# Performance work log

Hardware: AMD Instinct MI355X
Metric: run time of the kernel (lower is better)

The kernel has to match this reference:

```python
import jax, jax.numpy as jnp
import numpy as np
from jax import lax

B, S, T = 128, 1000, 256
V, E, KV, H = 30, 256, 256, 512


def setup_inputs() -> dict:
    ks = jax.random.split(jax.random.key(0), 20)
    sc = 0.1
    emb = jax.random.normal(ks[0], (V, E), jnp.float32) * sc
    emb = emb.at[29].set(0.0)  # padding_idx=29
    return {
        "enc_key": jax.random.normal(ks[1], (B, S, KV), jnp.float32),
        "value": jax.random.normal(ks[2], (B, S, KV), jnp.float32),
        "y": jax.random.randint(ks[3], (T, B), 0, V),
        "encoder_len": jax.random.randint(ks[4], (B,), 1, S + 1),
        "embedding": emb,
        "W_ih1": jax.random.normal(ks[5], (4 * H, E + KV), jnp.float32) * sc,
        "b_ih1": jax.random.normal(ks[6], (4 * H,), jnp.float32) * sc,
        "W_hh1": jax.random.normal(ks[7], (4 * H, H), jnp.float32) * sc,
        "b_hh1": jax.random.normal(ks[8], (4 * H,), jnp.float32) * sc,
        "W_ih2": jax.random.normal(ks[9], (4 * H, H), jnp.float32) * sc,
        "b_ih2": jax.random.normal(ks[10], (4 * H,), jnp.float32) * sc,
        "W_hh2": jax.random.normal(ks[11], (4 * H, H), jnp.float32) * sc,
        "b_hh2": jax.random.normal(ks[12], (4 * H,), jnp.float32) * sc,
        "Wq": jax.random.normal(ks[13], (KV, H), jnp.float32) * sc,
        "bq": jax.random.normal(ks[14], (KV,), jnp.float32) * sc,
        "Wc": jax.random.normal(ks[15], (V, 2 * KV), jnp.float32) * sc,
        "bc": jax.random.normal(ks[16], (V,), jnp.float32) * sc,
    }


def _lstm_cell(x, h, c, W_ih, b_ih, W_hh, b_hh):
    gates = x @ W_ih.T + b_ih + h @ W_hh.T + b_hh
    i, f, g, o = jnp.split(gates, 4, axis=1)
    c_new = jax.nn.sigmoid(f) * c + jax.nn.sigmoid(i) * jnp.tanh(g)
    h_new = jax.nn.sigmoid(o) * jnp.tanh(c_new)
    return h_new, c_new


def reference(enc_key, value, y, encoder_len, embedding,
              W_ih1, b_ih1, W_hh1, b_hh1,
              W_ih2, b_ih2, W_hh2, b_hh2,
              Wq, bq, Wc, bc):
    # y: [T, B] -> [B, T]; note: original computes mask from encoder_len but the
    # non-in-place masked_fill discards it, so masking has NO effect (reproduced).
    del encoder_len
    yT = y.T  # [B, T]
    b, s, kv = enc_key.shape
    scale = jnp.sqrt(jnp.asarray(s, jnp.float32))
    char_embeds = embedding[yT]          # [B, T, E]
    ctx0 = value.mean(axis=1)            # [B, KV]  (value.permute(0,2,1).mean(-1))
    h = W_hh1.shape[1]
    z = jnp.zeros((b, h), enc_key.dtype)

    def step(carry, e_t):
        h1, c1, h2, c2, ctx = carry
        x = jnp.concatenate([e_t, ctx], axis=1)                 # [B, E+KV]
        h1n, c1n = _lstm_cell(x, h1, c1, W_ih1, b_ih1, W_hh1, b_hh1)
        # original feeds lstm1's CELL state into lstm2 (hidden_states[0][1])
        h2n, c2n = _lstm_cell(c1n, h2, c2, W_ih2, b_ih2, W_hh2, b_hh2)
        # query from lstm2's CELL state (hidden_states[1][1])
        q = c2n @ Wq.T + bq                                     # [B, KV]
        energy = (jnp.einsum('bsk,bk->bs', enc_key, q) + 1e-9) / scale
        attn = jax.nn.softmax(energy, axis=1)                   # [B, S]
        ctxn = jnp.einsum('bsk,bs->bk', value, attn)            # [B, KV]
        pred = jnp.concatenate([ctxn, q], axis=1) @ Wc.T + bc   # [B, V]
        return (h1n, c1n, h2n, c2n, ctxn), (pred, attn[0])

    _, (preds, attn0) = lax.scan(step, (z, z, z, z, ctx0),
                                 jnp.swapaxes(char_embeds, 0, 1))
    predictions = jnp.transpose(preds, (1, 0, 2)).reshape(b, -1)  # [B, T*V] (cat dim=1)
    attentions = attn0[..., None]                                 # [T, S, 1]
    return predictions, attentions
```

## Files before the change

kernel.cpp:

```cpp
#include <hip/hip_runtime.h>
#include <hip/hip_bf16.h>

#define NB 128
#define NS 1000
#define NSH 500
#define NT 256
#define NV 30
#define NE 256
#define NKV 256
#define NH 512
#define NG 2048
#define NK 1024

typedef __hip_bfloat16 bf;
typedef unsigned short ushortT;

__device__ __forceinline__ float sigm(float x){ return 1.f/(1.f+__expf(-x)); }
__device__ __forceinline__ float tanh_fast(float x){ float e=__expf(2.f*x); return 1.f - 2.f/(e+1.f); }
__device__ __forceinline__ float bf2f(ushortT u){ return __uint_as_float(((unsigned)u)<<16); }
__device__ __forceinline__ void bf8_to_f(const ushortT* p, float* o){
  uint4 u = *reinterpret_cast<const uint4*>(p);
  o[0]=__uint_as_float(u.x<<16); o[1]=__uint_as_float(u.x&0xffff0000u);
  o[2]=__uint_as_float(u.y<<16); o[3]=__uint_as_float(u.y&0xffff0000u);
  o[4]=__uint_as_float(u.z<<16); o[5]=__uint_as_float(u.z&0xffff0000u);
  o[6]=__uint_as_float(u.w<<16); o[7]=__uint_as_float(u.w&0xffff0000u);
}
__device__ __forceinline__ float ldDual(const void* p, size_t i, bool bfm){
  return bfm ? bf2f(((const ushortT*)p)[i]) : ((const float*)p)[i];
}

__global__ void k_probe(const unsigned* __restrict__ x, unsigned* __restrict__ flag){
  __shared__ int cnt;
  if (threadIdx.x==0) cnt = 0;
  __syncthreads();
  int c = 0;
  #pragma unroll
  for (int i=0;i<4;++i){
    unsigned d = x[(size_t)threadIdx.x*4 + i];
    unsigned e = (d >> 7) & 0xffu;
    c += (e >= 119 && e <= 135) ? 1 : 0;
  }
  atomicAdd(&cnt, c);
  __syncthreads();
  if (threadIdx.x==0) *flag = (cnt >= 512) ? 1u : 0u;
}

__global__ void k_wtp(const void* __restrict__ A, const void* __restrict__ Bm,
                      float* __restrict__ Wtp, const unsigned* __restrict__ flag){
  const bool bfm = (*flag != 0);
  int idx = blockIdx.x*256 + threadIdx.x;
  int k = idx >> 11, pc = idx & (NG-1);
  int j = pc >> 2, g = pc & 3;
  int col = g*NH + j;
  const void* p = (k < NH) ? A : Bm;
  Wtp[idx] = ldDual(p, (size_t)col*NH + (k & (NH-1)), bfm);
}

__global__ void k_biasp(const void* bi1, const void* bh1, const void* bi2, const void* bh2,
                        float* __restrict__ bsum1, float* __restrict__ bsum2,
                        const unsigned* __restrict__ flag){
  const bool bfm = (*flag != 0);
  int idx = blockIdx.x*256 + threadIdx.x;
  int which = idx >= NG; int pc = idx & (NG-1);
  int j = pc >> 2, g = pc & 3;
  int col = g*NH + j;
  const void* a = which ? bi2 : bi1;
  const void* c = which ? bh2 : bh1;
  float v = ldDual(a, col, bfm) + ldDual(c, col, bfm);
  (which ? bsum2 : bsum1)[pc] = v;
}

__global__ void k_init(const void* __restrict__ value, const int* __restrict__ y,
                       const void* __restrict__ emb,
                       float* __restrict__ X1a, float* __restrict__ X2a,
                       float* __restrict__ c1, float* __restrict__ c2,
                       const unsigned* __restrict__ flag){
  const bool bfm = (*flag != 0);
  int b = blockIdx.x, tid = threadIdx.x;
  float acc = 0.f;
  if (bfm){
    const ushortT* vcol = (const ushortT*)value + (size_t)b*NS*NKV + tid;
    for (int s=0;s<NS;++s) acc += bf2f(vcol[(size_t)s*NKV]);
  } else {
    const float* vcol = (const float*)value + (size_t)b*NS*NKV + tid;
    for (int s=0;s<NS;++s) acc += vcol[(size_t)s*NKV];
  }
  X1a[(size_t)b*NK + NE + tid] = acc * (1.f/NS);
  int yv = y[b];
  X1a[(size_t)b*NK + tid] = ldDual(emb, (size_t)yv*NE + tid, bfm);
  X1a[(size_t)b*NK + 512 + tid] = 0.f; X1a[(size_t)b*NK + 768 + tid] = 0.f;
  X2a[(size_t)b*NK + 512 + tid] = 0.f; X2a[(size_t)b*NK + 768 + tid] = 0.f;
  c1[(size_t)b*NH + tid] = 0.f; c1[(size_t)b*NH + 256 + tid] = 0.f;
  c2[(size_t)b*NH + tid] = 0.f; c2[(size_t)b*NH + 256 + tid] = 0.f;
}

__global__ __launch_bounds__(512) void k_lstm(
    const float* __restrict__ X, const float* __restrict__ Wtp,
    const float* __restrict__ bsump,
    float* __restrict__ cstate,
    float* __restrict__ outC, int outCstride, int hasC,
    float* __restrict__ outH)
{
  const int i = blockIdx.x;
  const int cb = ((i & 7) << 3) | ((i >> 3) & 7);
  const int rb = i >> 6;
  const int r0 = rb * 32;
  const int pc0 = cb * 32;
  const int tid = threadIdx.x;
  const int khalf = tid >> 8;
  const int t8 = tid & 255;
  const int rp = t8 >> 4;
  const int cp = t8 & 15;
  __shared__ float Xs[2][64][33];
  __shared__ float redbuf[256][4];
  __shared__ float gbuf[32][33];

  float a00=0.f, a01=0.f, a10=0.f, a11=0.f;
  const int kbase = khalf * 512;
  const int sr  = t8 >> 4;
  const int sk4 = (t8 & 15) * 4;

  for (int cch = 0; cch < 8; ++cch){
    __syncthreads();
    {
      const float4 v0 = *reinterpret_cast<const float4*>(
          X + (size_t)(r0+sr)*NK + kbase + cch*64 + sk4);
      const float4 v1 = *reinterpret_cast<const float4*>(
          X + (size_t)(r0+sr+16)*NK + kbase + cch*64 + sk4);
      Xs[khalf][sk4+0][sr]    = v0.x; Xs[khalf][sk4+1][sr]    = v0.y;
      Xs[khalf][sk4+2][sr]    = v0.z; Xs[khalf][sk4+3][sr]    = v0.w;
      Xs[khalf][sk4+0][sr+16] = v1.x; Xs[khalf][sk4+1][sr+16] = v1.y;
      Xs[khalf][sk4+2][sr+16] = v1.z; Xs[khalf][sk4+3][sr+16] = v1.w;
    }
    __syncthreads();
    const float* wp = Wtp + (size_t)(kbase + cch*64)*NG + pc0 + cp*2;
    #pragma unroll 8
    for (int kk=0; kk<64; ++kk){
      const float2 w = *reinterpret_cast<const float2*>(wp + (size_t)kk*NG);
      const float2 x = *reinterpret_cast<const float2*>(&Xs[khalf][kk][rp*2]);
      a00 = fmaf(x.x, w.x, a00); a01 = fmaf(x.x, w.y, a01);
      a10 = fmaf(x.y, w.x, a10); a11 = fmaf(x.y, w.y, a11);
    }
  }
  if (khalf == 1){
    redbuf[t8][0]=a00; redbuf[t8][1]=a01; redbuf[t8][2]=a10; redbuf[t8][3]=a11;
  }
  __syncthreads();
  if (khalf == 0){
    a00 += redbuf[t8][0]; a01 += redbuf[t8][1];
    a10 += redbuf[t8][2]; a11 += redbuf[t8][3];
    gbuf[rp*2+0][cp*2+0]=a00; gbuf[rp*2+0][cp*2+1]=a01;
    gbuf[rp*2+1][cp*2+0]=a10; gbuf[rp*2+1][cp*2+1]=a11;
  }
  __syncthreads();
  if (tid < 256){
    const int er = tid >> 3;
    const int jj = tid & 7;
    const int r = r0 + er;
    const int jg = cb*8 + jj;
    const int pb = pc0 + jj*4;
    float iv = gbuf[er][jj*4+0] + bsump[pb+0];
    float fv = gbuf[er][jj*4+1] + bsump[pb+1];
    float gv = gbuf[er][jj*4+2] + bsump[pb+2];
    float ov = gbuf[er][jj*4+3] + bsump[pb+3];
    float cold = cstate[(size_t)r*NH + jg];
    float cn = sigm(fv)*cold + sigm(iv)*tanh_fast(gv);
    float hn = sigm(ov)*tanh_fast(cn);
    cstate[(size_t)r*NH + jg] = cn;
    if (hasC) outC[(size_t)r*outCstride + jg] = cn;
    outH[(size_t)r*NK + jg] = hn;
  }
}

__global__ __launch_bounds__(512) void k_attn_part(
    const float* __restrict__ c2, const void* __restrict__ Wq, const void* __restrict__ bq,
    const void* __restrict__ key, const void* __restrict__ val,
    float* __restrict__ qbuf, float* __restrict__ pctx, float* __restrict__ pstat,
    float* __restrict__ psbuf,
    const unsigned* __restrict__ flag)
{
  const bool bfm = (*flag != 0);
  const int b = blockIdx.x >> 1, half = blockIdx.x & 1;
  const int sbase = half * NSH;
  const int tid = threadIdx.x, lane = tid & 63, wave = tid >> 6;
  __shared__ float c2s[NH];
  __shared__ float qs[NKV];
  __shared__ float ps[512];
  __shared__ float red[16];
  __shared__ float ctxpart[8][NKV];

  c2s[tid] = c2[(size_t)b*NH + tid];
  __syncthreads();

  if (tid < NKV){
    float qacc = ldDual(bq, tid, bfm);
    if (bfm){
      const ushortT* wrow = (const ushortT*)Wq + (size_t)tid*NH;
      #pragma unroll 4
      for (int j=0;j<NH;j+=8){
        float wv[8]; bf8_to_f(wrow + j, wv);
        #pragma unroll
        for (int u=0;u<8;++u) qacc = fmaf(wv[u], c2s[j+u], qacc);
      }
    } else {
      const float4* wrow = reinterpret_cast<const float4*>((const float*)Wq + (size_t)tid*NH);
      #pragma unroll 4
      for (int j4=0; j4<NH/4; ++j4){
        float4 w = wrow[j4]; int j = j4*4;
        qacc = fmaf(w.x, c2s[j+0], qacc); qacc = fmaf(w.y, c2s[j+1], qacc);
        qacc = fmaf(w.z, c2s[j+2], qacc); qacc = fmaf(w.w, c2s[j+3], qacc);
      }
    }
    qs[tid] = qacc;
    if (half == 0) qbuf[(size_t)b*NKV + tid] = qacc;
  }
  __syncthreads();

  const int k0 = (lane & 15)*16;
  float qreg[16];
  #pragma unroll
  for (int u=0;u<16;++u) qreg[u] = qs[k0+u];
  const float rscale = 0.031622776601683794f;
  for (int i0 = wave*8; i0 < NSH; i0 += 64){
    int sA = i0 + (lane >> 4);
    int sB = sA + 4;
    float aA = 0.f, aB = 0.f;
    if (bfm){
      if (sA < NSH){
        const ushortT* kp = (const ushortT*)key + ((size_t)b*NS + sbase + sA)*NKV + k0;
        float xv[8];
        bf8_to_f(kp, xv);
        #pragma unroll
        for (int u=0;u<8;++u) aA = fmaf(xv[u], qreg[u], aA);
        bf8_to_f(kp + 8, xv);
        #pragma unroll
        for (int u=0;u<8;++u) aA = fmaf(xv[u], qreg[8+u], aA);
      }
      if (sB < NSH){
        const ushortT* kp = (const ushortT*)key + ((size_t)b*NS + sbase + sB)*NKV + k0;
        float xv[8];
        bf8_to_f(kp, xv);
        #pragma unroll
        for (int u=0;u<8;++u) aB = fmaf(xv[u], qreg[u], aB);
        bf8_to_f(kp + 8, xv);
        #pragma unroll
        for (int u=0;u<8;++u) aB = fmaf(xv[u], qreg[8+u], aB);
      }
    } else {
      const float* kA = (const float*)key + ((size_t)b*NS + sbase + sA)*NKV + k0;
      const float* kB = (const float*)key + ((size_t)b*NS + sbase + sB)*NKV + k0;
      float4 a0,a1,a2,a3, b0,b1,b2,b3;
      bool gA = (sA < NSH), gB = (sB < NSH);
      if (gA){
        a0 = *reinterpret_cast<const float4*>(kA);
        a1 = *reinterpret_cast<const float4*>(kA+4);
        a2 = *reinterpret_cast<const float4*>(kA+8);
        a3 = *reinterpret_cast<const float4*>(kA+12);
      }
      if (gB){
        b0 = *reinterpret_cast<const float4*>(kB);
        b1 = *reinterpret_cast<const float4*>(kB+4);
        b2 = *reinterpret_cast<const float4*>(kB+8);
        b3 = *reinterpret_cast<const float4*>(kB+12);
      }
      if (gA){
        aA = fmaf(a0.x,qreg[0],aA); aA = fmaf(a0.y,qreg[1],aA);
        aA = fmaf(a0.z,qreg[2],aA); aA = fmaf(a0.w,qreg[3],aA);
        aA = fmaf(a1.x,qreg[4],aA); aA = fmaf(a1.y,qreg[5],aA);
        aA = fmaf(a1.z,qreg[6],aA); aA = fmaf(a1.w,qreg[7],aA);
        aA = fmaf(a2.x,qreg[8],aA); aA = fmaf(a2.y,qreg[9],aA);
        aA = fmaf(a2.z,qreg[10],aA); aA = fmaf(a2.w,qreg[11],aA);
        aA = fmaf(a3.x,qreg[12],aA); aA = fmaf(a3.y,qreg[13],aA);
        aA = fmaf(a3.z,qreg[14],aA); aA = fmaf(a3.w,qreg[15],aA);
      }
      if (gB){
        aB = fmaf(b0.x,qreg[0],aB); aB = fmaf(b0.y,qreg[1],aB);
        aB = fmaf(b0.z,qreg[2],aB); aB = fmaf(b0.w,qreg[3],aB);
        aB = fmaf(b1.x,qreg[4],aB); aB = fmaf(b1.y,qreg[5],aB);
        aB = fmaf(b1.z,qreg[6],aB); aB = fmaf(b1.w,qreg[7],aB);
        aB = fmaf(b2.x,qreg[8],aB); aB = fmaf(b2.y,qreg[9],aB);
        aB = fmaf(b2.z,qreg[10],aB); aB = fmaf(b2.w,qreg[11],aB);
        aB = fmaf(b3.x,qreg[12],aB); aB = fmaf(b3.y,qreg[13],aB);
        aB = fmaf(b3.z,qreg[14],aB); aB = fmaf(b3.w,qreg[15],aB);
      }
    }
    aA += __shfl_xor(aA,1); aA += __shfl_xor(aA,2);
    aA += __shfl_xor(aA,4); aA += __shfl_xor(aA,8);
    aB += __shfl_xor(aB,1); aB += __shfl_xor(aB,2);
    aB += __shfl_xor(aB,4); aB += __shfl_xor(aB,8);
    if ((lane & 15) == 0){
      if (sA < NSH) ps[sA] = (aA + 1e-9f)*rscale;
      if (sB < NSH) ps[sB] = (aB + 1e-9f)*rscale;
    }
  }
  __syncthreads();

  float m = -1e30f;
  if (tid < NSH) m = ps[tid];
  #pragma unroll
  for (int d=1; d<64; d<<=1) m = fmaxf(m, __shfl_xor(m, d));
  if (lane == 0) red[wave] = m;
  __syncthreads();
  m = red[0];
  #pragma unroll
  for (int w=1; w<8; ++w) m = fmaxf(m, red[w]);
  float sum = 0.f;
  if (tid < NSH){ float p = __expf(ps[tid]-m); ps[tid] = p; sum = p; }
  #pragma unroll
  for (int d=1; d<64; d<<=1) sum += __shfl_xor(sum, d);
  if (lane == 0) red[8+wave] = sum;
  __syncthreads();
  sum = red[8];
  #pragma unroll
  for (int w=1; w<8; ++w) sum += red[8+w];
  if (tid == 0){
    pstat[((size_t)b*2 + half)*2 + 0] = m;
    pstat[((size_t)b*2 + half)*2 + 1] = sum;
  }
  if (b == 0 && tid < NSH) psbuf[sbase + tid] = ps[tid];

  {
    float ca[8] = {0.f,0.f,0.f,0.f,0.f,0.f,0.f,0.f};
    float cb2[8] = {0.f,0.f,0.f,0.f,0.f,0.f,0.f,0.f};
    const int sset = lane >> 5;
    const int kc = (lane & 31) * 8;
    const int sst = wave*2 + sset;
    int s = sst;
    if (bfm){
      const ushortT* vbase = (const ushortT*)val + ((size_t)b*NS + sbase)*NKV + kc;
      for (; s + 16 < NSH; s += 32){
        float p0 = ps[s], p1 = ps[s+16];
        float xv[8];
        bf8_to_f(vbase + (size_t)s*NKV, xv);
        #pragma unroll
        for (int u=0;u<8;++u) ca[u] = fmaf(xv[u], p0, ca[u]);
        bf8_to_f(vbase + (size_t)(s+16)*NKV, xv);
        #pragma unroll
        for (int u=0;u<8;++u) cb2[u] = fmaf(xv[u], p1, cb2[u]);
      }
      if (s < NSH){
        float p0 = ps[s];
        float xv[8]; bf8_to_f(vbase + (size_t)s*NKV, xv);
        #pragma unroll
        for (int u=0;u<8;++u) ca[u] = fmaf(xv[u], p0, ca[u]);
      }
    } else {
      const float* vbase = (const float*)val + ((size_t)b*NS + sbase)*NKV + kc;
      for (; s + 16 < NSH; s += 32){
        float p0 = ps[s], p1 = ps[s+16];
        const float4 v0 = *reinterpret_cast<const float4*>(vbase + (size_t)s*NKV);
        const float4 v1 = *reinterpret_cast<const float4*>(vbase + (size_t)s*NKV + 4);
        const float4 w0 = *reinterpret_cast<const float4*>(vbase + (size_t)(s+16)*NKV);
        const float4 w1 = *reinterpret_cast<const float4*>(vbase + (size_t)(s+16)*NKV + 4);
        ca[0]=fmaf(v0.x,p0,ca[0]); ca[1]=fmaf(v0.y,p0,ca[1]);
        ca[2]=fmaf(v0.z,p0,ca[2]); ca[3]=fmaf(v0.w,p0,ca[3]);
        ca[4]=fmaf(v1.x,p0,ca[4]); ca[5]=fmaf(v1.y,p0,ca[5]);
        ca[6]=fmaf(v1.z,p0,ca[6]); ca[7]=fmaf(v1.w,p0,ca[7]);
        cb2[0]=fmaf(w0.x,p1,cb2[0]); cb2[1]=fmaf(w0.y,p1,cb2[1]);
        cb2[2]=fmaf(w0.z,p1,cb2[2]); cb2[3]=fmaf(w0.w,p1,cb2[3]);
        cb2[4]=fmaf(w1.x,p1,cb2[4]); cb2[5]=fmaf(w1.y,p1,cb2[5]);
        cb2[6]=fmaf(w1.z,p1,cb2[6]); cb2[7]=fmaf(w1.w,p1,cb2[7]);
      }
      if (s < NSH){
        float p0 = ps[s];
        const float4 v0 = *reinterpret_cast<const float4*>(vbase + (size_t)s*NKV);
        const float4 v1 = *reinterpret_cast<const float4*>(vbase + (size_t)s*NKV + 4);
        ca[0]=fmaf(v0.x,p0,ca[0]); ca[1]=fmaf(v0.y,p0,ca[1]);
        ca[2]=fmaf(v0.z,p0,ca[2]); ca[3]=fmaf(v0.w,p0,ca[3]);
        ca[4]=fmaf(v1.x,p0,ca[4]); ca[5]=fmaf(v1.y,p0,ca[5]);
        ca[6]=fmaf(v1.z,p0,ca[6]); ca[7]=fmaf(v1.w,p0,ca[7]);
      }
    }
    #pragma unroll
    for (int u=0;u<8;++u){
      float v = ca[u] + cb2[u];
      v += __shfl_xor(v, 32);
      if (lane < 32) ctxpart[wave][kc+u] = v;
    }
  }
  __syncthreads();
  if (tid < NKV){
    float ctxv = 0.f;
    #pragma unroll
    for (int w=0; w<8; ++w) ctxv += ctxpart[w][tid];
    pctx[((size_t)b*2 + half)*NKV + tid] = ctxv;
  }
}

__global__ __launch_bounds__(256) void k_attn_comb(
    const float* __restrict__ qbuf, const float* __restrict__ pctx,
    const float* __restrict__ pstat, const float* __restrict__ psbuf,
    const void* __restrict__ Wc, const void* __restrict__ bc,
    const int* __restrict__ y, const void* __restrict__ emb,
    float* __restrict__ X1next, void* __restrict__ outp,
    const unsigned* __restrict__ flag, int t)
{
  const bool bfm = (*flag != 0);
  const int b = blockIdx.x, tid = threadIdx.x;
  __shared__ float qs[NKV];
  __shared__ float ctxs[NKV];
  __shared__ float psum[NV][9];

  const float mA = pstat[((size_t)b*2+0)*2+0], sA = pstat[((size_t)b*2+0)*2+1];
  const float mB = pstat[((size_t)b*2+1)*2+0], sB = pstat[((size_t)b*2+1)*2+1];
  const float m = fmaxf(mA, mB);
  const float wA = __expf(mA - m), wB = __expf(mB - m);
  const float invS = 1.f / (sA*wA + sB*wB);

  qs[tid] = qbuf[(size_t)b*NKV + tid];
  float ctxv = (pctx[((size_t)b*2+0)*NKV + tid]*wA +
                pctx[((size_t)b*2+1)*NKV + tid]*wB) * invS;
  ctxs[tid] = ctxv;
  X1next[(size_t)b*NK + NE + tid] = ctxv;

  const size_t ATTN_OFF = (size_t)NB*NT*NV;
  if (b == 0){
    for (int s=tid; s<NS; s+=256){
      float v = psbuf[s] * ((s < NSH) ? wA : wB) * invS;
      if (bfm) ((bf*)outp)[ATTN_OFF + (size_t)t*NS + s] = __float2bfloat16(v);
      else     ((float*)outp)[ATTN_OFF + (size_t)t*NS + s] = v;
    }
  }
  __syncthreads();

  {
    int vIdx = tid >> 3, part = tid & 7;
    if (vIdx < NV){
      float a = 0.f;
      int kb0 = part*64;
      for (int k=kb0; k<kb0+64; ++k){
        float xv = (k < NKV) ? ctxs[k] : qs[k-NKV];
        a = fmaf(xv, ldDual(Wc, (size_t)vIdx*(2*NKV) + k, bfm), a);
      }
      psum[vIdx][part] = a;
    }
  }
  __syncthreads();
  if (tid < NV){
    float a = ldDual(bc, tid, bfm);
    #pragma unroll
    for (int p=0;p<8;++p) a += psum[tid][p];
    size_t oi = (size_t)b*(NT*NV) + (size_t)t*NV + tid;
    if (bfm) ((bf*)outp)[oi] = __float2bfloat16(a);
    else     ((float*)outp)[oi] = a;
  }

  if (t + 1 < NT){
    int yv = y[(size_t)(t+1)*NB + b];
    X1next[(size_t)b*NK + tid] = ldDual(emb, (size_t)yv*NE + tid, bfm);
  }
}

extern "C" void kernel_launch(void* const* d_in, const int* in_sizes, int n_in,
                              void* d_out, int out_size, void* d_ws, size_t ws_size,
                              hipStream_t stream)
{
  const void* enc_key = d_in[0];
  const void* value   = d_in[1];
  const int*  y       = (const int*)d_in[2];
  const void* emb     = d_in[4];
  const void* W_ih1   = d_in[5];
  const void* b_ih1   = d_in[6];
  const void* W_hh1   = d_in[7];
  const void* b_hh1   = d_in[8];
  const void* W_ih2   = d_in[9];
  const void* b_ih2   = d_in[10];
  const void* W_hh2   = d_in[11];
  const void* b_hh2   = d_in[12];
  const void* Wq      = d_in[13];
  const void* bq      = d_in[14];
  const void* Wc      = d_in[15];
  const void* bc      = d_in[16];

  char* base = (char*)d_ws; size_t off = 0;
  auto alloc = [&](size_t bytes)->char*{
    char* p = base + off; off += (bytes + 255) & ~(size_t)255; return p;
  };
  float* Wtp1 = (float*)alloc((size_t)NK*NG*4);
  float* Wtp2 = (float*)alloc((size_t)NK*NG*4);
  float* bsum1 = (float*)alloc((size_t)NG*4);
  float* bsum2 = (float*)alloc((size_t)NG*4);
  float* X1[2] = {(float*)alloc((size_t)NB*NK*4), (float*)alloc((size_t)NB*NK*4)};
  float* X2[2] = {(float*)alloc((size_t)NB*NK*4), (float*)alloc((size_t)NB*NK*4)};
  float* c1 = (float*)alloc((size_t)NB*NH*4);
  float* c2 = (float*)alloc((size_t)NB*NH*4);
  float* qbuf  = (float*)alloc((size_t)NB*NKV*4);
  float* pctx  = (float*)alloc((size_t)NB*2*NKV*4);
  float* pstat = (float*)alloc((size_t)NB*2*2*4);
  float* psbuf = (float*)alloc((size_t)NS*4);
  unsigned* flag = (unsigned*)alloc(256);
  (void)ws_size;

  k_probe<<<1, 256, 0, stream>>>((const unsigned*)enc_key, flag);
  k_wtp<<<(NK*NG)/256, 256, 0, stream>>>(W_ih1, W_hh1, Wtp1, flag);
  k_wtp<<<(NK*NG)/256, 256, 0, stream>>>(W_ih2, W_hh2, Wtp2, flag);
  k_biasp<<<(2*NG)/256, 256, 0, stream>>>(b_ih1, b_hh1, b_ih2, b_hh2, bsum1, bsum2, flag);
  k_init<<<NB, 256, 0, stream>>>(value, y, emb, X1[0], X2[0], c1, c2, flag);

  for (int t=0; t<NT; ++t){
    int cur = t & 1, nxt = cur ^ 1;
    k_lstm<<<256, 512, 0, stream>>>(X1[cur], Wtp1, bsum1, c1,
                                    X2[cur], NK, 1, X1[nxt] + NH);
    k_lstm<<<256, 512, 0, stream>>>(X2[cur], Wtp2, bsum2, c2,
                                    nullptr, 0, 0, X2[nxt] + NH);
    k_attn_part<<<2*NB, 512, 0, stream>>>(c2, Wq, bq, enc_key, value,
                                          qbuf, pctx, pstat, psbuf, flag);
    k_attn_comb<<<NB, 256, 0, stream>>>(qbuf, pctx, pstat, psbuf, Wc, bc,
                                        y, emb, X1[nxt], d_out, flag, t);
  }
}
```

Measured before the change: 38.53 ms.

## Fuse attention combine into partial kernel via last-block atomic counter

Merges the attention combine kernel into the split-S attention kernel. Each of the two half-blocks per batch row increments a per-step atomic counter, and the second finisher merges the partial softmax stats, context and prediction. This removes one kernel launch per timestep (256 launches) and the qbuf round trip, at the cost of threadfences, an atomic, and a zeroed counter buffer sized per step.

```diff
diff --git a/kernel.cpp b/kernel.cpp
--- a/kernel.cpp
+++ b/kernel.cpp
@@ -43,6 +43,11 @@
   atomicAdd(&cnt, c);
   __syncthreads();
   if (threadIdx.x==0) *flag = (cnt >= 512) ? 1u : 0u;
+}
+
+__global__ void k_zero(unsigned* __restrict__ p, int n){
+  int i = blockIdx.x*256 + threadIdx.x;
+  if (i < n) p[i] = 0u;
 }
 
 __global__ void k_wtp(const void* __restrict__ A, const void* __restrict__ Bm,
@@ -172,12 +177,15 @@
   }
 }
 
-__global__ __launch_bounds__(512) void k_attn_part(
+__global__ __launch_bounds__(512) void k_attn(
     const float* __restrict__ c2, const void* __restrict__ Wq, const void* __restrict__ bq,
     const void* __restrict__ key, const void* __restrict__ val,
-    float* __restrict__ qbuf, float* __restrict__ pctx, float* __restrict__ pstat,
-    float* __restrict__ psbuf,
-    const unsigned* __restrict__ flag)
+    float* __restrict__ pctx, float* __restrict__ pstat, float* __restrict__ psbuf,
+    unsigned* __restrict__ cnt,
+    const void* __restrict__ Wc, const void* __restrict__ bc,
+    const int* __restrict__ y, const void* __restrict__ emb,
+    float* __restrict__ X1next, void* __restrict__ outp,
+    const unsigned* __restrict__ flag, int t)
 {
   const bool bfm = (*flag != 0);
   const int b = blockIdx.x >> 1, half = blockIdx.x & 1;
@@ -188,6 +196,9 @@
   __shared__ float ps[512];
   __shared__ float red[16];
   __shared__ float ctxpart[8][NKV];
+  __shared__ float ctxs[NKV];
+  __shared__ float psum[NV][9];
+  __shared__ unsigned oldv;
 
   c2s[tid] = c2[(size_t)b*NH + tid];
   __syncthreads();
@@ -212,7 +223,6 @@
       }
     }
     qs[tid] = qacc;
-    if (half == 0) qbuf[(size_t)b*NKV + tid] = qacc;
   }
   __syncthreads();
 
@@ -250,20 +260,20 @@
       const float* kA = (const float*)key + ((size_t)b*NS + sbase + sA)*NKV + k0;
       const float* kB = (const float*)key + ((size_t)b*NS + sbase + sB)*NKV + k0;
       float4 a0,a1,a2,a3, b0,b1,b2,b3;
-      bool gA = (sA < NSH), gB = (sB < NSH);
-      if (gA){
+      bool okA = (sA < NSH), okB = (sB < NSH);
+      if (okA){
         a0 = *reinterpret_cast<const float4*>(kA);
         a1 = *reinterpret_cast<const float4*>(kA+4);
         a2 = *reinterpret_cast<const float4*>(kA+8);
         a3 = *reinterpret_cast<const float4*>(kA+12);
       }
-      if (gB){
+      if (okB){
         b0 = *reinterpret_cast<const float4*>(kB);
         b1 = *reinterpret_cast<const float4*>(kB+4);
         b2 = *reinterpret_cast<const float4*>(kB+8);
         b3 = *reinterpret_cast<const float4*>(kB+12);
       }
-      if (gA){
+      if (okA){
         aA = fmaf(a0.x,qreg[0],aA); aA = fmaf(a0.y,qreg[1],aA);
         aA = fmaf(a0.z,qreg[2],aA); aA = fmaf(a0.w,qreg[3],aA);
         aA = fmaf(a1.x,qreg[4],aA); aA = fmaf(a1.y,qreg[5],aA);
@@ -273,7 +283,7 @@
         aA = fmaf(a3.x,qreg[12],aA); aA = fmaf(a3.y,qreg[13],aA);
         aA = fmaf(a3.z,qreg[14],aA); aA = fmaf(a3.w,qreg[15],aA);
       }
-      if (gB){
+      if (okB){
         aB = fmaf(b0.x,qreg[0],aB); aB = fmaf(b0.y,qreg[1],aB);
         aB = fmaf(b0.z,qreg[2],aB); aB = fmaf(b0.w,qreg[3],aB);
         aB = fmaf(b1.x,qreg[4],aB); aB = fmaf(b1.y,qreg[5],aB);
@@ -385,36 +395,29 @@
     for (int w=0; w<8; ++w) ctxv += ctxpart[w][tid];
     pctx[((size_t)b*2 + half)*NKV + tid] = ctxv;
   }
-}
-
-__global__ __launch_bounds__(256) void k_attn_comb(
-    const float* __restrict__ qbuf, const float* __restrict__ pctx,
-    const float* __restrict__ pstat, const float* __restrict__ psbuf,
-    const void* __restrict__ Wc, const void* __restrict__ bc,
-    const int* __restrict__ y, const void* __restrict__ emb,
-    float* __restrict__ X1next, void* __restrict__ outp,
-    const unsigned* __restrict__ flag, int t)
-{
-  const bool bfm = (*flag != 0);
-  const int b = blockIdx.x, tid = threadIdx.x;
-  __shared__ float qs[NKV];
-  __shared__ float ctxs[NKV];
-  __shared__ float psum[NV][9];
+  __syncthreads();
+
+  __threadfence();
+  if (tid == 0) oldv = atomicAdd(&cnt[b], 1u);
+  __syncthreads();
+  if (oldv != 1u) return;
+  __threadfence();
 
   const float mA = pstat[((size_t)b*2+0)*2+0], sA = pstat[((size_t)b*2+0)*2+1];
   const float mB = pstat[((size_t)b*2+1)*2+0], sB = pstat[((size_t)b*2+1)*2+1];
-  const float m = fmaxf(mA, mB);
-  const float wA = __expf(mA - m), wB = __expf(mB - m);
+  const float mm = fmaxf(mA, mB);
+  const float wA = __expf(mA - mm), wB = __expf(mB - mm);
   const float invS = 1.f / (sA*wA + sB*wB);
 
-  qs[tid] = qbuf[(size_t)b*NKV + tid];
-  float ctxv = (pctx[((size_t)b*2+0)*NKV + tid]*wA +
-                pctx[((size_t)b*2+1)*NKV + tid]*wB) * invS;
-  ctxs[tid] = ctxv;
-  X1next[(size_t)b*NK + NE + tid] = ctxv;
+  if (tid < NKV){
+    float ctxv = (pctx[((size_t)b*2+0)*NKV + tid]*wA +
+                  pctx[((size_t)b*2+1)*NKV + tid]*wB) * invS;
+    ctxs[tid] = ctxv;
+    X1next[(size_t)b*NK + NE + tid] = ctxv;
+  }
 
   const size_t ATTN_OFF = (size_t)NB*NT*NV;
-  if (b == 0){
+  if (b == 0 && tid < 256){
     for (int s=tid; s<NS; s+=256){
       float v = psbuf[s] * ((s < NSH) ? wA : wB) * invS;
       if (bfm) ((bf*)outp)[ATTN_OFF + (size_t)t*NS + s] = __float2bfloat16(v);
@@ -423,7 +426,7 @@
   }
   __syncthreads();
 
-  {
+  if (tid < 256){
     int vIdx = tid >> 3, part = tid & 7;
     if (vIdx < NV){
       float a = 0.f;
@@ -445,7 +448,7 @@
     else     ((float*)outp)[oi] = a;
   }
 
-  if (t + 1 < NT){
+  if (t + 1 < NT && tid < NE){
     int yv = y[(size_t)(t+1)*NB + b];
     X1next[(size_t)b*NK + tid] = ldDual(emb, (size_t)yv*NE + tid, bfm);
   }
@@ -484,14 +487,15 @@
   float* X2[2] = {(float*)alloc((size_t)NB*NK*4), (float*)alloc((size_t)NB*NK*4)};
   float* c1 = (float*)alloc((size_t)NB*NH*4);
   float* c2 = (float*)alloc((size_t)NB*NH*4);
-  float* qbuf  = (float*)alloc((size_t)NB*NKV*4);
   float* pctx  = (float*)alloc((size_t)NB*2*NKV*4);
   float* pstat = (float*)alloc((size_t)NB*2*2*4);
   float* psbuf = (float*)alloc((size_t)NS*4);
+  unsigned* cntbuf = (unsigned*)alloc((size_t)NT*NB*4);
   unsigned* flag = (unsigned*)alloc(256);
   (void)ws_size;
 
   k_probe<<<1, 256, 0, stream>>>((const unsigned*)enc_key, flag);
+  k_zero<<<(NT*NB+255)/256, 256, 0, stream>>>(cntbuf, NT*NB);
   k_wtp<<<(NK*NG)/256, 256, 0, stream>>>(W_ih1, W_hh1, Wtp1, flag);
   k_wtp<<<(NK*NG)/256, 256, 0, stream>>>(W_ih2, W_hh2, Wtp2, flag);
   k_biasp<<<(2*NG)/256, 256, 0, stream>>>(b_ih1, b_hh1, b_ih2, b_hh2, bsum1, bsum2, flag);
@@ -503,9 +507,8 @@
                                     X2[cur], NK, 1, X1[nxt] + NH);
     k_lstm<<<256, 512, 0, stream>>>(X2[cur], Wtp2, bsum2, c2,
                                     nullptr, 0, 0, X2[nxt] + NH);
-    k_attn_part<<<2*NB, 512, 0, stream>>>(c2, Wq, bq, enc_key, value,
-                                          qbuf, pctx, pstat, psbuf, flag);
-    k_attn_comb<<<NB, 256, 0, stream>>>(qbuf, pctx, pstat, psbuf, Wc, bc,
-                                        y, emb, X1[nxt], d_out, flag, t);
-  }
-}
+    k_attn<<<2*NB, 512, 0, stream>>>(c2, Wq, bq, enc_key, value,
+                                     pctx, pstat, psbuf, cntbuf + (size_t)t*NB,
+                                     Wc, bc, y, emb, X1[nxt], d_out, flag, t);
+  }
+}
```

Result: slower. 62.63 ms (+62.5%).
